# Kernel optimization log

Measured on AMD Instinct MI355X. Metric: run time of the kernel, lower is better.

## Reference

```python
import jax, jax.numpy as jnp
import numpy as np

# ---- dims / hyperparams (match init_kwargs) ----
D, B, S, NE, NC = 256, 4, 8192, 2048, 512
WIN, RK, TKE, TKC = 4, 4, 4, 4          # s window, route_topk, expanded_topk, compressed_topk
ALPHA, BS2B, BB2S = 1.0, 0.5, 0.5       # alpha_b, beta_s_to_b, beta_b_to_s
S_SC, B_SC, X_SC = 0.25, 0.2, 0.15      # s/b/cross delta scales
EPS = 1e-5
INV_SQRT_D = float(1.0 / np.sqrt(D))


def _ln(x, g, b):
    m = jnp.mean(x, -1, keepdims=True)
    v = jnp.mean(jnp.square(x - m), -1, keepdims=True)
    return (x - m) * jax.lax.rsqrt(v + EPS) * g + b


def _window_prop(state, val, w):
    # local window attention via diagonal-bilinear pairwise scores; never builds [S,S]
    n = state.shape[1]
    offs = jnp.arange(-WIN, WIN + 1)
    idx = jnp.arange(n)[:, None] + offs[None, :]            # [n, K]
    valid = (idx >= 0) & (idx < n)
    idxc = jnp.clip(idx, 0, n - 1)
    nb_s = state[:, idxc]                                    # [B, n, K, D]
    nb_v = val[:, idxc]
    sc = jnp.einsum('bnd,bnkd->bnk', state * w, nb_s) * INV_SQRT_D
    sc = jnp.where(valid, sc, -1e30)
    a = jax.nn.softmax(sc, axis=-1)
    return (jnp.einsum('bnk,bnkd->bnd', a, nb_s),
            jnp.einsum('bnk,bnkd->bnd', a, nb_v))


def _topk_prop(state, val, w, k):
    # global topk sparse attention over the (small) expanded/compressed node set
    sc = jnp.einsum('bnd,bmd->bnm', state * w, state) * INV_SQRT_D
    top, idx = jax.lax.top_k(sc, k)                          # [B, N, k]
    a = jax.nn.softmax(top, axis=-1)
    take = jax.vmap(lambda x, i: x[i])                       # gather rows per batch
    nb_s = take(state, idx)                                  # [B, N, k, D]
    nb_v = take(val, idx)
    return (jnp.einsum('bnk,bnkd->bnd', a, nb_s),
            jnp.einsum('bnk,bnkd->bnd', a, nb_v))


def _sparse_transition(src_s, src_v, W, bias, nd, k):
    # LinearRoute logits -> topk dst per src -> softmax weights -> scatter-add into dst
    logits = src_s @ W + bias                                # [B, Ns, Nd]
    top, idx = jax.lax.top_k(logits, k)
    wgt = jax.nn.softmax(top, axis=-1)                       # [B, Ns, k]

    def scat(i, ww, fs, fv):
        ii = i.reshape(-1)
        cs = (ww[..., None] * fs[:, None, :]).reshape(-1, fs.shape[-1])
        cv = (ww[..., None] * fv[:, None, :]).reshape(-1, fv.shape[-1])
        z = jnp.zeros((nd, fs.shape[-1]), fs.dtype)
        return z.at[ii].add(cs), z.at[ii].add(cv)

    return jax.vmap(scat)(idx, wgt, src_s, src_v)            # [B, Nd, D] x2


def _forward(s_state, s_val, w_pair_s, w_pair_e, w_pair_c,
             W_expand, b_expand, W_b2s, b_b2s, W_comp, b_comp, W_s2b, b_s2b,
             ln_g_s, ln_b_s, ln_g_e, ln_b_e, ln_g_c, ln_b_c):
    bsz = s_state.shape[0]
    # 1) sequence window propagation + stabilize
    ds, dv = _window_prop(s_state, s_val, w_pair_s)
    s_state = jnp.tanh(s_state + S_SC * ds)
    s_val = _ln(s_val + S_SC * dv, ln_g_s, ln_b_s)
    # 2) compressed layer bootstrapped from zeros (compressed_b=None) + stabilize
    c_state = jnp.zeros((bsz, NC, D), s_state.dtype)
    c_val = _ln(jnp.zeros((bsz, NC, D), s_state.dtype), ln_g_c, ln_b_c)
    # 3) expanded layer: expand transition then topk propagation + stabilize
    e_state = jnp.zeros((bsz, NE, D), s_state.dtype)
    e_val = jnp.zeros((bsz, NE, D), s_state.dtype)
    sc_b = ALPHA * B_SC
    ds, dv = _sparse_transition(c_state, c_val, W_expand, b_expand, NE, RK)
    e_state = e_state + sc_b * ds; e_val = e_val + sc_b * dv
    ds, dv = _topk_prop(e_state, e_val, w_pair_e, TKE)
    e_state = jnp.tanh(e_state + sc_b * ds)
    e_val = _ln(e_val + sc_b * dv, ln_g_e, ln_b_e)
    # 4) expanded -> sequence cross update + stabilize
    sc_x = ALPHA * BB2S * X_SC
    ds, dv = _sparse_transition(e_state, e_val, W_b2s, b_b2s, S, RK)
    s_state = jnp.tanh(s_state + sc_x * ds)
    s_val = _ln(s_val + sc_x * dv, ln_g_s, ln_b_s)
    # 5) next compressed: compress, s->b, compressed propagation + stabilize
    nc_state, nc_val = c_state, c_val
    ds, dv = _sparse_transition(e_state, e_val, W_comp, b_comp, NC, RK)
    nc_state = nc_state + sc_b * ds; nc_val = nc_val + sc_b * dv
    sc_sb = ALPHA * BS2B * X_SC
    ds, dv = _sparse_transition(s_state, s_val, W_s2b, b_s2b, NC, RK)
    nc_state = nc_state + sc_sb * ds; nc_val = nc_val + sc_sb * dv
    ds, dv = _topk_prop(nc_state, nc_val, w_pair_c, TKC)
    nc_state = jnp.tanh(nc_state + sc_b * ds)
    nc_val = _ln(nc_val + sc_b * dv, ln_g_c, ln_b_c)
    return (s_state, s_val, nc_state, nc_val)


def setup_inputs() -> dict:
    key = jax.random.key(0)
    ks = jax.random.split(key, 16)
    rs = float(1.0 / np.sqrt(D))
    return {
        's_state': jax.random.normal(ks[0], (B, S, D), jnp.float32),
        's_val': jax.random.normal(ks[1], (B, S, D), jnp.float32),
        'w_pair_s': jax.random.normal(ks[2], (D,), jnp.float32) * rs,
        'w_pair_e': jax.random.normal(ks[3], (D,), jnp.float32) * rs,
        'w_pair_c': jax.random.normal(ks[4], (D,), jnp.float32) * rs,
        'W_expand': jax.random.normal(ks[5], (D, NE), jnp.float32) * rs,
        'b_expand': jnp.zeros((NE,), jnp.float32),
        'W_b2s': jax.random.normal(ks[6], (D, S), jnp.float32) * rs,
        'b_b2s': jnp.zeros((S,), jnp.float32),
        'W_comp': jax.random.normal(ks[7], (D, NC), jnp.float32) * rs,
        'b_comp': jnp.zeros((NC,), jnp.float32),
        'W_s2b': jax.random.normal(ks[8], (D, NC), jnp.float32) * rs,
        'b_s2b': jnp.zeros((NC,), jnp.float32),
        'ln_g_s': jnp.ones((D,), jnp.float32), 'ln_b_s': jnp.zeros((D,), jnp.float32),
        'ln_g_e': jnp.ones((D,), jnp.float32), 'ln_b_e': jnp.zeros((D,), jnp.float32),
        'ln_g_c': jnp.ones((D,), jnp.float32), 'ln_b_c': jnp.zeros((D,), jnp.float32),
    }


def reference(s_state, s_val, w_pair_s, w_pair_e, w_pair_c,
              W_expand, b_expand, W_b2s, b_b2s, W_comp, b_comp, W_s2b, b_s2b,
              ln_g_s, ln_b_s, ln_g_e, ln_b_e, ln_g_c, ln_b_c):
    return _forward(s_state, s_val, w_pair_s, w_pair_e, w_pair_c,
                    W_expand, b_expand, W_b2s, b_b2s, W_comp, b_comp, W_s2b, b_s2b,
                    ln_g_s, ln_b_s, ln_g_e, ln_b_e, ln_g_c, ln_b_c)
```

## Files before the change

kernel.cpp:

```cpp
#include <hip/hip_runtime.h>
#include <math.h>

#define DD 256
#define BATCH 4
#define SEQ 8192
#define NEE 2048
#define NCC 512
#define EPSL 1e-5f
#define INV_SQRT_D 0.0625f

typedef __attribute__((ext_vector_type(8))) short short8;
typedef __attribute__((ext_vector_type(4))) float f32x4;

__device__ __forceinline__ float4 ld4(const float* p){ return *(const float4*)p; }
__device__ __forceinline__ void st4(float* p, const float4& v){ *(float4*)p = v; }
__device__ __forceinline__ void fma4(float4& a, float s, const float4& b){
  a.x = fmaf(s,b.x,a.x); a.y = fmaf(s,b.y,a.y); a.z = fmaf(s,b.z,a.z); a.w = fmaf(s,b.w,a.w);
}
__device__ __forceinline__ float4 tanh4(const float4& v){
  float4 r; r.x=tanhf(v.x); r.y=tanhf(v.y); r.z=tanhf(v.z); r.w=tanhf(v.w); return r;
}
__device__ __forceinline__ ushort f2bf(float x){
  unsigned u = __float_as_uint(x);
  unsigned r = u + 0x7fffu + ((u >> 16) & 1u);
  return (ushort)(r >> 16);
}
__device__ __forceinline__ float bf2f(ushort h){
  return __uint_as_float(((unsigned)h) << 16);
}

__device__ __forceinline__ bool t4_better(float v1, int i1, float v2, int i2){
  return (v1 > v2) || (v1 == v2 && i1 < i2);
}
__device__ __forceinline__ void t4_init(float* v, int* i){
#pragma unroll
  for (int k=0;k<4;k++){ v[k] = -INFINITY; i[k] = 0x7fffffff; }
}
__device__ __forceinline__ void t4_insert(float* v, int* i, float nv, int ni){
  if (t4_better(nv, ni, v[3], i[3])){
    v[3]=nv; i[3]=ni;
    if (t4_better(v[3],i[3],v[2],i[2])){ float tv=v[2]; v[2]=v[3]; v[3]=tv; int ti=i[2]; i[2]=i[3]; i[3]=ti;
      if (t4_better(v[2],i[2],v[1],i[1])){ tv=v[1]; v[1]=v[2]; v[2]=tv; ti=i[1]; i[1]=i[2]; i[2]=ti;
        if (t4_better(v[1],i[1],v[0],i[0])){ tv=v[0]; v[0]=v[1]; v[1]=tv; ti=i[0]; i[0]=i[1]; i[1]=ti; }
      }
    }
  }
}
__device__ __forceinline__ void t4_ce(float* v, int* i, int x, int y){
  if (t4_better(v[y],i[y],v[x],i[x])){ float tv=v[x]; v[x]=v[y]; v[y]=tv; int ti=i[x]; i[x]=i[y]; i[y]=ti; }
}
__device__ __forceinline__ void t4_merge(float* av, int* ai, const float* bv, const int* bi){
  float lv[4]; int li[4];
#pragma unroll
  for (int k=0;k<4;k++){
    if (t4_better(av[k],ai[k],bv[3-k],bi[3-k])){ lv[k]=av[k]; li[k]=ai[k]; }
    else { lv[k]=bv[3-k]; li[k]=bi[3-k]; }
  }
  t4_ce(lv,li,0,2); t4_ce(lv,li,1,3); t4_ce(lv,li,0,1); t4_ce(lv,li,2,3);
#pragma unroll
  for (int k=0;k<4;k++){ av[k]=lv[k]; ai[k]=li[k]; }
}
__device__ __forceinline__ void t4_wave_merge(float* v, int* i){
#pragma unroll
  for (int off=1; off<64; off<<=1){
    float bv[4]; int bi[4];
#pragma unroll
    for (int k=0;k<4;k++){ bv[k]=__shfl_xor(v[k],off); bi[k]=__shfl_xor(i[k],off); }
    t4_merge(v,i,bv,bi);
  }
}

__global__ __launch_bounds__(256) void k0_prep(
    const float* __restrict__ b_expand, const float* __restrict__ b_b2s, const float* __restrict__ b_comp,
    const float* __restrict__ ln_b_c, const float* __restrict__ ln_g_e, const float* __restrict__ ln_b_e,
    float* __restrict__ sumE, int* __restrict__ idxB2S, float* __restrict__ wgtB2S,
    int* __restrict__ idxComp, float* __restrict__ wgtComp)
{
  __shared__ int s_idx[3][4];
  __shared__ float s_wgt[3][4];
  __shared__ float red[16];
  int t = threadIdx.x, wv = t>>6, lane = t&63;
  if (wv < 3){
    const float* arr = (wv==0)? b_expand : (wv==1? b_b2s : b_comp);
    int n = (wv==0)? NEE : (wv==1? SEQ : NCC);
    float v[4]; int ix[4]; t4_init(v,ix);
    for (int m=lane; m<n; m+=64) t4_insert(v,ix, arr[m], m);
    t4_wave_merge(v,ix);
    if (lane==0){
      float e0=1.f, e1=expf(v[1]-v[0]), e2=expf(v[2]-v[0]), e3=expf(v[3]-v[0]);
      float inv = 1.f/(e0+e1+e2+e3);
      s_idx[wv][0]=ix[0]; s_idx[wv][1]=ix[1]; s_idx[wv][2]=ix[2]; s_idx[wv][3]=ix[3];
      s_wgt[wv][0]=e0*inv; s_wgt[wv][1]=e1*inv; s_wgt[wv][2]=e2*inv; s_wgt[wv][3]=e3*inv;
    }
  }
  __syncthreads();
  float c = ln_b_c[t];
  float cs = c, cq = c*c;
#pragma unroll
  for (int off=32; off; off>>=1){ cs += __shfl_xor(cs,off); cq += __shfl_xor(cq,off); }
  if (lane==0){ red[wv]=cs; red[8+wv]=cq; }
  __syncthreads();
  float mean_c = (red[0]+red[1]+red[2]+red[3]) * (1.f/256.f);
  float var_c  = (red[8]+red[9]+red[10]+red[11]) * (1.f/256.f) - mean_c*mean_c;
  float cm = c - mean_c;
  float g = ln_g_e[t], be = ln_b_e[t];
  float a[4]; float q = 0.f;
#pragma unroll
  for (int k=0;k<4;k++){
    a[k] = 0.2f * (float)NCC * s_wgt[0][k];
    if (s_idx[0][k] < 4) q += a[k];
  }
  q *= 0.25f;
  float se = 0.f;
#pragma unroll
  for (int k=0;k<4;k++){
    float tk = a[k] + 0.2f*q;
    se += tk*cm*rsqrtf(tk*tk*var_c + EPSL)*g + be;
  }
  float tz = 0.2f*q;
  se += (float)(NEE-4) * (tz*cm*rsqrtf(tz*tz*var_c + EPSL)*g + be);
  sumE[t] = se;
  if (t < 4){
    idxB2S[t] = s_idx[1][t]; wgtB2S[t] = s_wgt[1][t];
    idxComp[t] = s_idx[2][t]; wgtComp[t] = s_wgt[2][t];
  }
}

__global__ __launch_bounds__(256) void k1_window(
    const float* __restrict__ s_state, const float* __restrict__ s_val,
    const float* __restrict__ w_pair_s, const float* __restrict__ ln_g_s, const float* __restrict__ ln_b_s,
    const float* __restrict__ sumE, const int* __restrict__ idxB2S, const float* __restrict__ wgtB2S,
    float* __restrict__ out_state, float* __restrict__ out_val)
{
  int gw = (blockIdx.x << 2) + (threadIdx.x >> 6);
  int lane = threadIdx.x & 63;
  int b = gw >> 13, r = gw & (SEQ-1);
  size_t rowoff = ((size_t)gw) << 8;
  size_t bbase = ((size_t)b) << 21;
  int d0 = lane << 2;
  float4 x = ld4(s_state + rowoff + d0);
  float4 v = ld4(s_val + rowoff + d0);
  float4 wp = ld4(w_pair_s + d0);
  float qx=x.x*wp.x, qy=x.y*wp.y, qz=x.z*wp.z, qw=x.w*wp.w;
  float sc[9]; float4 ns[9];
#pragma unroll
  for (int k=0;k<9;k++){
    int rr = r + k - 4;
    int rc = rr < 0 ? 0 : (rr > SEQ-1 ? SEQ-1 : rr);
    ns[k] = ld4(s_state + bbase + (((size_t)rc)<<8) + d0);
    sc[k] = qx*ns[k].x + qy*ns[k].y + qz*ns[k].z + qw*ns[k].w;
  }
#pragma unroll
  for (int off=32; off; off>>=1){
#pragma unroll
    for (int k=0;k<9;k++) sc[k] += __shfl_xor(sc[k], off);
  }
  float mx = -INFINITY;
#pragma unroll
  for (int k=0;k<9;k++){
    int rr = r + k - 4;
    sc[k] = (rr>=0 && rr<SEQ) ? sc[k]*INV_SQRT_D : -1e30f;
    mx = fmaxf(mx, sc[k]);
  }
  float ssum = 0.f;
#pragma unroll
  for (int k=0;k<9;k++){ sc[k] = expf(sc[k]-mx); ssum += sc[k]; }
  float inv = 1.f/ssum;
  float4 ds = make_float4(0,0,0,0), dv = make_float4(0,0,0,0);
#pragma unroll
  for (int k=0;k<9;k++) fma4(ds, sc[k]*inv, ns[k]);
#pragma unroll
  for (int k=0;k<9;k++){
    int rr = r + k - 4;
    int rc = rr < 0 ? 0 : (rr > SEQ-1 ? SEQ-1 : rr);
    float4 nv = ld4(s_val + bbase + (((size_t)rc)<<8) + d0);
    fma4(dv, sc[k]*inv, nv);
  }
  float4 s1;
  s1.x = tanhf(x.x + 0.25f*ds.x); s1.y = tanhf(x.y + 0.25f*ds.y);
  s1.z = tanhf(x.z + 0.25f*ds.z); s1.w = tanhf(x.w + 0.25f*ds.w);
  st4(out_state + rowoff + d0, tanh4(s1));
  float4 y;
  y.x = v.x + 0.25f*dv.x; y.y = v.y + 0.25f*dv.y; y.z = v.z + 0.25f*dv.z; y.w = v.w + 0.25f*dv.w;
  float sm = y.x+y.y+y.z+y.w;
  float sq = y.x*y.x+y.y*y.y+y.z*y.z+y.w*y.w;
#pragma unroll
  for (int off=32; off; off>>=1){ sm += __shfl_xor(sm,off); sq += __shfl_xor(sq,off); }
  float mean = sm*(1.f/256.f);
  float rstd = rsqrtf(sq*(1.f/256.f) - mean*mean + EPSL);
  float4 g = ld4(ln_g_s + d0), be = ld4(ln_b_s + d0);
  float4 y1;
  y1.x = (y.x-mean)*rstd*g.x + be.x; y1.y = (y.y-mean)*rstd*g.y + be.y;
  y1.z = (y.z-mean)*rstd*g.z + be.z; y1.w = (y.w-mean)*rstd*g.w + be.w;
#pragma unroll
  for (int k=0;k<4;k++){
    if (r == idxB2S[k]){
      float cb = 0.075f * wgtB2S[k];
      float4 sE = ld4(sumE + d0);
      fma4(y1, cb, sE);
    }
  }
  sm = y1.x+y1.y+y1.z+y1.w;
  sq = y1.x*y1.x+y1.y*y1.y+y1.z*y1.z+y1.w*y1.w;
#pragma unroll
  for (int off=32; off; off>>=1){ sm += __shfl_xor(sm,off); sq += __shfl_xor(sq,off); }
  float mean2 = sm*(1.f/256.f);
  float rstd2 = rsqrtf(sq*(1.f/256.f) - mean2*mean2 + EPSL);
  float4 o;
  o.x = (y1.x-mean2)*rstd2*g.x + be.x; o.y = (y1.y-mean2)*rstd2*g.y + be.y;
  o.z = (y1.z-mean2)*rstd2*g.z + be.z; o.w = (y1.w-mean2)*rstd2*g.w + be.w;
  st4(out_val + rowoff + d0, o);
}

__global__ __launch_bounds__(256) void k2w_pack(const float* __restrict__ W,
    ushort* __restrict__ Whi, ushort* __restrict__ Wlo)
{
  int t = blockIdx.x*256 + threadIdx.x;
  int kb = t >> 11;
  int cf = (t >> 6) & 31;
  int l  = t & 63;
  int k0 = kb*32 + ((l>>4)<<3);
  int col = (cf<<4) + (l&15);
  size_t off = (size_t)t << 3;
#pragma unroll
  for (int j=0;j<8;j++){
    float x = W[(size_t)(k0+j)*NCC + col];
    ushort h = f2bf(x);
    Whi[off+j] = h;
    Wlo[off+j] = f2bf(x - bf2f(h));
  }
}

__global__ __launch_bounds__(256) void k2_mfma(
    const float* __restrict__ A, const ushort* __restrict__ Whi, const ushort* __restrict__ Wlo,
    const float* __restrict__ bias,
    int* __restrict__ topk_idx, float* __restrict__ topk_wgt, int* __restrict__ counts)
{
  __shared__ __align__(16) ushort Asp[2][32][264];
  __shared__ float mv[32][17];
  __shared__ int   mi[32][17];
  int tid = threadIdx.x;
  size_t row_base = (size_t)blockIdx.x * 32;
  {
    const float4* Ab = (const float4*)(A + row_base*DD);
#pragma unroll
    for (int i=0;i<8;i++){
      int q = i*256 + tid;
      int row = q >> 6, k4 = q & 63;
      float4 x = Ab[q];
      ushort4 h, lo;
      h.x = f2bf(x.x); h.y = f2bf(x.y); h.z = f2bf(x.z); h.w = f2bf(x.w);
      lo.x = f2bf(x.x - bf2f(h.x)); lo.y = f2bf(x.y - bf2f(h.y));
      lo.z = f2bf(x.z - bf2f(h.z)); lo.w = f2bf(x.w - bf2f(h.w));
      *(ushort4*)&Asp[0][row][k4*4] = h;
      *(ushort4*)&Asp[1][row][k4*4] = lo;
    }
  }
  __syncthreads();
  int w = tid >> 6, l = tid & 63;
  int lg = l >> 4, lr = l & 15;
  f32x4 acc[2][8];
#pragma unroll
  for (int rf=0; rf<2; rf++)
#pragma unroll
    for (int cf=0; cf<8; cf++) acc[rf][cf] = (f32x4){0.f,0.f,0.f,0.f};
  for (int kb=0; kb<8; kb++){
    short8 bh[8], bl[8];
#pragma unroll
    for (int cf=0; cf<8; cf++){
      int cfg = (w<<3) + cf;
      size_t off = (((size_t)(kb*32 + cfg) << 6) + l) << 3;
      bh[cf] = *(const short8*)(Whi + off);
      bl[cf] = *(const short8*)(Wlo + off);
    }
    short8 ah[2], al[2];
#pragma unroll
    for (int rf=0; rf<2; rf++){
      int row = (rf<<4) + lr;
      int k = kb*32 + (lg<<3);
      ah[rf] = *(const short8*)&Asp[0][row][k];
      al[rf] = *(const short8*)&Asp[1][row][k];
    }
#pragma unroll
    for (int cf=0; cf<8; cf++){
#pragma unroll
      for (int rf=0; rf<2; rf++){
        acc[rf][cf] = __builtin_amdgcn_mfma_f32_16x16x32_bf16(ah[rf], bh[cf], acc[rf][cf], 0, 0, 0);
        acc[rf][cf] = __builtin_amdgcn_mfma_f32_16x16x32_bf16(al[rf], bh[cf], acc[rf][cf], 0, 0, 0);
        acc[rf][cf] = __builtin_amdgcn_mfma_f32_16x16x32_bf16(ah[rf], bl[cf], acc[rf][cf], 0, 0, 0);
      }
    }
  }
  float bcol[8];
  int rel[8];
#pragma unroll
  for (int cf=0; cf<8; cf++){
    bcol[cf] = bias[(w<<7) + (cf<<4) + lr];
    rel[cf] = (cf<<4) + lr;
  }
#pragma unroll
  for (int rf=0; rf<2; rf++){
#pragma unroll
    for (int reg=0; reg<4; reg++){
      float av[8];
#pragma unroll
      for (int cf=0; cf<8; cf++) av[cf] = acc[rf][cf][reg] + bcol[cf];
      float tv4[4]; int tc4[4];
#pragma unroll
      for (int r=0; r<4; r++){
        float m = fmaxf(fmaxf(fmaxf(av[0],av[1]),fmaxf(av[2],av[3])),
                        fmaxf(fmaxf(av[4],av[5]),fmaxf(av[6],av[7])));
#pragma unroll
        for (int off=1; off<16; off<<=1) m = fmaxf(m, __shfl_xor(m, off));
        int cand = 0x7fffffff;
#pragma unroll
        for (int cf=7; cf>=0; cf--) cand = (av[cf]==m) ? rel[cf] : cand;
#pragma unroll
        for (int off=1; off<16; off<<=1) cand = min(cand, __shfl_xor(cand, off));
        tv4[r] = m; tc4[r] = cand;
        if (r < 3){
#pragma unroll
          for (int cf=0; cf<8; cf++) av[cf] = (rel[cf]==cand) ? -INFINITY : av[cf];
        }
      }
      if (lr == 0){
        int rowl = (rf<<4) + (lg<<2) + reg;
#pragma unroll
        for (int r=0; r<4; r++){ mv[rowl][(w<<2)+r] = tv4[r]; mi[rowl][(w<<2)+r] = (w<<7) + tc4[r]; }
      }
    }
  }
  __syncthreads();
  if (tid < 32){
    float v[4]; int ix[4]; t4_init(v, ix);
#pragma unroll
    for (int j=0; j<16; j++) t4_insert(v, ix, mv[tid][j], mi[tid][j]);
    float e0=1.f, e1=expf(v[1]-v[0]), e2=expf(v[2]-v[0]), e3=expf(v[3]-v[0]);
    float inv = 1.f/(e0+e1+e2+e3);
    size_t row = row_base + tid;
    int b = (int)(row >> 13);
    topk_idx[row*4+0]=ix[0]; topk_idx[row*4+1]=ix[1]; topk_idx[row*4+2]=ix[2]; topk_idx[row*4+3]=ix[3];
    topk_wgt[row*4+0]=e0*inv; topk_wgt[row*4+1]=e1*inv; topk_wgt[row*4+2]=e2*inv; topk_wgt[row*4+3]=e3*inv;
    atomicAdd(&counts[(b<<9)+ix[0]],1); atomicAdd(&counts[(b<<9)+ix[1]],1);
    atomicAdd(&counts[(b<<9)+ix[2]],1); atomicAdd(&counts[(b<<9)+ix[3]],1);
  }
}

__global__ void kz_zero(int* __restrict__ counts){
  int i = blockIdx.x*256 + threadIdx.x;
  if (i < BATCH*NCC) counts[i] = 0;
}

__global__ __launch_bounds__(256) void k3_scan(const int* __restrict__ counts,
    int* __restrict__ offsets, int* __restrict__ cursor)
{
  __shared__ int part[256];
  int t = threadIdx.x;
  int loc[8]; int s = 0;
#pragma unroll
  for (int i=0;i<8;i++){ loc[i] = counts[t*8+i]; s += loc[i]; }
  part[t] = s;
  __syncthreads();
  for (int off=1; off<256; off<<=1){
    int add = (t>=off)? part[t-off] : 0;
    __syncthreads();
    part[t] += add;
    __syncthreads();
  }
  int run = part[t] - s;
#pragma unroll
  for (int i=0;i<8;i++){ offsets[t*8+i] = run; cursor[t*8+i] = run; run += loc[i]; }
  if (t==255) offsets[BATCH*NCC] = run;
}

__global__ void k4_fill(const int* __restrict__ topk_idx, const float* __restrict__ topk_wgt,
    int* __restrict__ cursor, int* __restrict__ csr_src, float* __restrict__ csr_wgt)
{
  int row = blockIdx.x*256 + threadIdx.x;
  if (row >= BATCH*SEQ) return;
  int b = row >> 13, r = row & (SEQ-1);
#pragma unroll
  for (int k=0;k<4;k++){
    int dest = topk_idx[row*4+k];
    float wgt = topk_wgt[row*4+k];
    int pos = atomicAdd(&cursor[(b<<9)+dest], 1);
    csr_src[pos] = r;
    csr_wgt[pos] = 0.075f * wgt;
  }
}

__global__ __launch_bounds__(256) void k5_gather(
    const int* __restrict__ offsets, const int* __restrict__ csr_src, const float* __restrict__ csr_wgt,
    const float* __restrict__ st, const float* __restrict__ vl,
    const float* __restrict__ ln_b_c, const float* __restrict__ sumE,
    const int* __restrict__ idxComp, const float* __restrict__ wgtComp,
    float* __restrict__ ncs, float* __restrict__ ncv)
{
  int g = blockIdx.x;
  int b = g >> 9, dest = g & (NCC-1);
  int t = threadIdx.x;
  int i0 = offsets[g], i1 = offsets[g+1];
  const float* Sb = st + (((size_t)b)<<21);
  const float* Vb = vl + (((size_t)b)<<21);
  float accs = 0.f, accv = 0.f;
  for (int i=i0; i<i1; i++){
    int src = csr_src[i];
    float wg = csr_wgt[i];
    accs = fmaf(wg, Sb[((size_t)src<<8) + t], accs);
    accv = fmaf(wg, Vb[((size_t)src<<8) + t], accv);
  }
  float base = ln_b_c[t];
#pragma unroll
  for (int k=0;k<4;k++) if (dest == idxComp[k]) base = fmaf(0.2f*wgtComp[k], sumE[t], base);
  ncs[((size_t)g<<8) + t] = accs;
  ncv[((size_t)g<<8) + t] = base + accv;
}

__global__ __launch_bounds__(256) void k5t_transpose(const float* __restrict__ ncs, float* __restrict__ ncsT){
  __shared__ float tile[64][65];
  int b = blockIdx.z;
  int m0 = blockIdx.x*64, d0 = blockIdx.y*64;
  int tx = threadIdx.x & 63, ty = threadIdx.x >> 6;
  const float* src = ncs + (((size_t)b)<<17);
  for (int i=ty; i<64; i+=4) tile[i][tx] = src[(size_t)(m0+i)*DD + d0 + tx];
  __syncthreads();
  float* dst = ncsT + (((size_t)b)<<17);
  for (int i=ty; i<64; i+=4) dst[(size_t)(d0+i)*NCC + m0 + tx] = tile[tx][i];
}

__global__ __launch_bounds__(256) void k6_ncprop(
    const float* __restrict__ ncs, const float* __restrict__ ncv, const float* __restrict__ ncsT,
    const float* __restrict__ w_pair_c, const float* __restrict__ ln_g_c, const float* __restrict__ ln_b_c,
    float* __restrict__ o_ncs, float* __restrict__ o_ncv)
{
  __shared__ float Alds[256*13];
  int tid = threadIdx.x;
  int b = blockIdx.x >> 6;
  int n_base = (blockIdx.x & 63) << 3;
  const float* Sb = ncs + (((size_t)b)<<17);
  const float* Vb = ncv + (((size_t)b)<<17);
  const float* Tb = ncsT + (((size_t)b)<<17);
  float wc = w_pair_c[tid] * INV_SQRT_D;
#pragma unroll
  for (int i=0;i<8;i++) Alds[tid*13 + i] = Sb[(size_t)(n_base+i)*DD + tid] * wc;
  __syncthreads();
  int lane = tid & 63, rg = tid >> 6;
  int r0 = rg << 1, c0 = lane << 3;
  float acc[2][8];
#pragma unroll
  for (int j=0;j<2;j++)
#pragma unroll
    for (int c=0;c<8;c++) acc[j][c] = 0.f;
  for (int kk=0; kk<256; kk++){
    float4 w0 = ld4(Tb + (size_t)kk*NCC + c0);
    float4 w1 = ld4(Tb + (size_t)kk*NCC + c0 + 4);
    float a0 = Alds[kk*13 + r0];
    float a1 = Alds[kk*13 + r0 + 1];
    float wv_[8] = {w0.x,w0.y,w0.z,w0.w,w1.x,w1.y,w1.z,w1.w};
#pragma unroll
    for (int c=0;c<8;c++){
      acc[0][c] = fmaf(a0, wv_[c], acc[0][c]);
      acc[1][c] = fmaf(a1, wv_[c], acc[1][c]);
    }
  }
  int d0 = lane << 2;
  float4 g4 = ld4(ln_g_c + d0), be4 = ld4(ln_b_c + d0);
#pragma unroll
  for (int j=0;j<2;j++){
    float tv[4]; int ti[4]; t4_init(tv,ti);
#pragma unroll
    for (int c=0;c<8;c++) t4_insert(tv,ti, acc[j][c], c0+c);
    t4_wave_merge(tv,ti);
    float e0=1.f, e1=expf(tv[1]-tv[0]), e2=expf(tv[2]-tv[0]), e3=expf(tv[3]-tv[0]);
    float inv = 1.f/(e0+e1+e2+e3);
    float aw[4] = {e0*inv, e1*inv, e2*inv, e3*inv};
    int n = n_base + r0 + j;
    float4 stt = ld4(Sb + (size_t)n*DD + d0);
    float4 vv  = ld4(Vb + (size_t)n*DD + d0);
    float4 dsv = make_float4(0,0,0,0), dvv = make_float4(0,0,0,0);
#pragma unroll
    for (int k=0;k<4;k++){
      float4 ms = ld4(Sb + (size_t)ti[k]*DD + d0);
      float4 mv = ld4(Vb + (size_t)ti[k]*DD + d0);
      fma4(dsv, aw[k], ms); fma4(dvv, aw[k], mv);
    }
    float4 os;
    os.x = tanhf(stt.x + 0.2f*dsv.x); os.y = tanhf(stt.y + 0.2f*dsv.y);
    os.z = tanhf(stt.z + 0.2f*dsv.z); os.w = tanhf(stt.w + 0.2f*dsv.w);
    size_t orow = (((size_t)b)<<17) + ((size_t)n<<8);
    st4(o_ncs + orow + d0, os);
    float4 y;
    y.x = vv.x + 0.2f*dvv.x; y.y = vv.y + 0.2f*dvv.y;
    y.z = vv.z + 0.2f*dvv.z; y.w = vv.w + 0.2f*dvv.w;
    float sm = y.x+y.y+y.z+y.w;
    float sq = y.x*y.x+y.y*y.y+y.z*y.z+y.w*y.w;
#pragma unroll
    for (int off=32; off; off>>=1){ sm += __shfl_xor(sm,off); sq += __shfl_xor(sq,off); }
    float mean = sm*(1.f/256.f);
    float rstd = rsqrtf(sq*(1.f/256.f) - mean*mean + EPSL);
    float4 o;
    o.x = (y.x-mean)*rstd*g4.x + be4.x; o.y = (y.y-mean)*rstd*g4.y + be4.y;
    o.z = (y.z-mean)*rstd*g4.z + be4.z; o.w = (y.w-mean)*rstd*g4.w + be4.w;
    st4(o_ncv + orow + d0, o);
  }
}

extern "C" void kernel_launch(void* const* d_in, const int* in_sizes, int n_in,
                              void* d_out, int out_size, void* d_ws, size_t ws_size,
                              hipStream_t stream)
{
  const float* s_state = (const float*)d_in[0];
  const float* s_val   = (const float*)d_in[1];
  const float* w_pair_s= (const float*)d_in[2];
  const float* w_pair_c= (const float*)d_in[4];
  const float* b_expand= (const float*)d_in[6];
  const float* b_b2s   = (const float*)d_in[8];
  const float* b_comp  = (const float*)d_in[10];
  const float* W_s2b   = (const float*)d_in[11];
  const float* b_s2b   = (const float*)d_in[12];
  const float* ln_g_s  = (const float*)d_in[13];
  const float* ln_b_s  = (const float*)d_in[14];
  const float* ln_g_e  = (const float*)d_in[15];
  const float* ln_b_e  = (const float*)d_in[16];
  const float* ln_g_c  = (const float*)d_in[17];
  const float* ln_b_c  = (const float*)d_in[18];

  float* o_sstate = (float*)d_out;
  float* o_sval   = o_sstate + (size_t)BATCH*SEQ*DD;
  float* o_ncs    = o_sval + (size_t)BATCH*SEQ*DD;
  float* o_ncv    = o_ncs + (size_t)BATCH*NCC*DD;

  char* w = (char*)d_ws;
  float* sumE    = (float*)(w);
  int*   idxB2S  = (int*)(w + 1024);
  float* wgtB2S  = (float*)(w + 1040);
  int*   idxComp = (int*)(w + 1056);
  float* wgtComp = (float*)(w + 1072);
  int*   topk_idx= (int*)(w + 4096);
  float* topk_wgt= (float*)(w + 4096 + 524288);
  int*   counts  = (int*)(w + 1052672);
  int*   offsets = (int*)(w + 1069056);
  int*   cursor  = (int*)(w + 1085440);
  int*   csr_src = (int*)(w + 1101824);
  float* csr_wgt = (float*)(w + 1626112);
  float* ncs_ws  = (float*)(w + 2150400);
  float* ncv_ws  = ncs_ws + (size_t)BATCH*NCC*DD;
  float* ncsT_ws = ncv_ws + (size_t)BATCH*NCC*DD;
  ushort* wpk_hi = (ushort*)(w + 8441856);
  ushort* wpk_lo = (ushort*)(w + 8441856 + 262144);

  hipLaunchKernelGGL(k0_prep, dim3(1), dim3(256), 0, stream,
      b_expand, b_b2s, b_comp, ln_b_c, ln_g_e, ln_b_e, sumE, idxB2S, wgtB2S, idxComp, wgtComp);
  hipLaunchKernelGGL(k2w_pack, dim3(64), dim3(256), 0, stream, W_s2b, wpk_hi, wpk_lo);
  hipLaunchKernelGGL(k1_window, dim3(8192), dim3(256), 0, stream,
      s_state, s_val, w_pair_s, ln_g_s, ln_b_s, sumE, idxB2S, wgtB2S, o_sstate, o_sval);
  hipLaunchKernelGGL(kz_zero, dim3(8), dim3(256), 0, stream, counts);
  hipLaunchKernelGGL(k2_mfma, dim3(1024), dim3(256), 0, stream,
      o_sstate, wpk_hi, wpk_lo, b_s2b, topk_idx, topk_wgt, counts);
  hipLaunchKernelGGL(k3_scan, dim3(1), dim3(256), 0, stream, counts, offsets, cursor);
  hipLaunchKernelGGL(k4_fill, dim3(128), dim3(256), 0, stream,
      topk_idx, topk_wgt, cursor, csr_src, csr_wgt);
  hipLaunchKernelGGL(k5_gather, dim3(2048), dim3(256), 0, stream,
      offsets, csr_src, csr_wgt, o_sstate, o_sval, ln_b_c, sumE, idxComp, wgtComp, ncs_ws, ncv_ws);
  hipLaunchKernelGGL(k5t_transpose, dim3(8,4,BATCH), dim3(256), 0, stream, ncs_ws, ncsT_ws);
  hipLaunchKernelGGL(k6_ncprop, dim3(256), dim3(256), 0, stream,
      ncs_ws, ncv_ws, ncsT_ws, w_pair_c, ln_g_c, ln_b_c, o_ncs, o_ncv);
}
```

Measured before the change: 417.3 us.

## Software-pipeline W fragment loads in k2_mfma with register double buffering

Restructures the k2_mfma inner loop so the packed hi/lo weight fragments are fetched in groups of two column tiles into alternating register buffers. The next group's global loads are issued before the current group's MFMAs, with sched_barrier fencing the order. The first group is prefetched before the A-tile conversion, and the lo weights are addressed by a fixed offset from the hi pointer instead of a separate argument. A launch_bounds occupancy hint of 4 is added to cap register use, which risks spilling or scheduling constraints in exchange for hiding global load latency behind matrix ops.

```diff
diff --git a/kernel.cpp b/kernel.cpp
--- a/kernel.cpp
+++ b/kernel.cpp
@@ -231,8 +231,8 @@
   }
 }
 
-__global__ __launch_bounds__(256) void k2_mfma(
-    const float* __restrict__ A, const ushort* __restrict__ Whi, const ushort* __restrict__ Wlo,
+__global__ __launch_bounds__(256, 4) void k2_mfma(
+    const float* __restrict__ A, const ushort* __restrict__ Whi,
     const float* __restrict__ bias,
     int* __restrict__ topk_idx, float* __restrict__ topk_wgt, int* __restrict__ counts)
 {
@@ -241,6 +241,34 @@
   __shared__ int   mi[32][17];
   int tid = threadIdx.x;
   size_t row_base = (size_t)blockIdx.x * 32;
+  int w = tid >> 6, l = tid & 63;
+  int lg = l >> 4, lr = l & 15;
+  const ushort* pw = Whi + ((w<<12) + (l<<3));
+
+#define LOADG(KB, G, DST) { \
+    const ushort* _p = pw + (KB)*16384 + (G)*1024; \
+    DST[0] = *(const short8*)_p; \
+    DST[2] = *(const short8*)(_p + 512); \
+    DST[1] = *(const short8*)(_p + 131072); \
+    DST[3] = *(const short8*)(_p + 131072 + 512); }
+
+#define COMPG(G, B) { \
+    int _c0 = (G)<<1, _c1 = _c0+1; \
+    acc[0][_c0] = __builtin_amdgcn_mfma_f32_16x16x32_bf16(ah0, B[0], acc[0][_c0], 0,0,0); \
+    acc[1][_c0] = __builtin_amdgcn_mfma_f32_16x16x32_bf16(ah1, B[0], acc[1][_c0], 0,0,0); \
+    acc[0][_c1] = __builtin_amdgcn_mfma_f32_16x16x32_bf16(ah0, B[2], acc[0][_c1], 0,0,0); \
+    acc[1][_c1] = __builtin_amdgcn_mfma_f32_16x16x32_bf16(ah1, B[2], acc[1][_c1], 0,0,0); \
+    acc[0][_c0] = __builtin_amdgcn_mfma_f32_16x16x32_bf16(al0, B[0], acc[0][_c0], 0,0,0); \
+    acc[1][_c0] = __builtin_amdgcn_mfma_f32_16x16x32_bf16(al1, B[0], acc[1][_c0], 0,0,0); \
+    acc[0][_c0] = __builtin_amdgcn_mfma_f32_16x16x32_bf16(ah0, B[1], acc[0][_c0], 0,0,0); \
+    acc[1][_c0] = __builtin_amdgcn_mfma_f32_16x16x32_bf16(ah1, B[1], acc[1][_c0], 0,0,0); \
+    acc[0][_c1] = __builtin_amdgcn_mfma_f32_16x16x32_bf16(al0, B[2], acc[0][_c1], 0,0,0); \
+    acc[1][_c1] = __builtin_amdgcn_mfma_f32_16x16x32_bf16(al1, B[2], acc[1][_c1], 0,0,0); \
+    acc[0][_c1] = __builtin_amdgcn_mfma_f32_16x16x32_bf16(ah0, B[3], acc[0][_c1], 0,0,0); \
+    acc[1][_c1] = __builtin_amdgcn_mfma_f32_16x16x32_bf16(ah1, B[3], acc[1][_c1], 0,0,0); }
+
+  short8 bA[4], bB[4];
+  LOADG(0, 0, bA);
   {
     const float4* Ab = (const float4*)(A + row_base*DD);
 #pragma unroll
@@ -257,40 +285,33 @@
     }
   }
   __syncthreads();
-  int w = tid >> 6, l = tid & 63;
-  int lg = l >> 4, lr = l & 15;
   f32x4 acc[2][8];
 #pragma unroll
   for (int rf=0; rf<2; rf++)
 #pragma unroll
     for (int cf=0; cf<8; cf++) acc[rf][cf] = (f32x4){0.f,0.f,0.f,0.f};
+#pragma unroll 1
   for (int kb=0; kb<8; kb++){
-    short8 bh[8], bl[8];
-#pragma unroll
-    for (int cf=0; cf<8; cf++){
-      int cfg = (w<<3) + cf;
-      size_t off = (((size_t)(kb*32 + cfg) << 6) + l) << 3;
-      bh[cf] = *(const short8*)(Whi + off);
-      bl[cf] = *(const short8*)(Wlo + off);
-    }
-    short8 ah[2], al[2];
-#pragma unroll
-    for (int rf=0; rf<2; rf++){
-      int row = (rf<<4) + lr;
-      int k = kb*32 + (lg<<3);
-      ah[rf] = *(const short8*)&Asp[0][row][k];
-      al[rf] = *(const short8*)&Asp[1][row][k];
-    }
-#pragma unroll
-    for (int cf=0; cf<8; cf++){
-#pragma unroll
-      for (int rf=0; rf<2; rf++){
-        acc[rf][cf] = __builtin_amdgcn_mfma_f32_16x16x32_bf16(ah[rf], bh[cf], acc[rf][cf], 0, 0, 0);
-        acc[rf][cf] = __builtin_amdgcn_mfma_f32_16x16x32_bf16(al[rf], bh[cf], acc[rf][cf], 0, 0, 0);
-        acc[rf][cf] = __builtin_amdgcn_mfma_f32_16x16x32_bf16(ah[rf], bl[cf], acc[rf][cf], 0, 0, 0);
-      }
-    }
-  }
+    int ka = kb*32 + (lg<<3);
+    short8 ah0 = *(const short8*)&Asp[0][lr][ka];
+    short8 ah1 = *(const short8*)&Asp[0][16+lr][ka];
+    short8 al0 = *(const short8*)&Asp[1][lr][ka];
+    short8 al1 = *(const short8*)&Asp[1][16+lr][ka];
+    LOADG(kb, 1, bB);
+    __builtin_amdgcn_sched_barrier(0);
+    COMPG(0, bA);
+    LOADG(kb, 2, bA);
+    __builtin_amdgcn_sched_barrier(0);
+    COMPG(1, bB);
+    LOADG(kb, 3, bB);
+    __builtin_amdgcn_sched_barrier(0);
+    COMPG(2, bA);
+    if (kb < 7) LOADG(kb+1, 0, bA);
+    __builtin_amdgcn_sched_barrier(0);
+    COMPG(3, bB);
+  }
+#undef LOADG
+#undef COMPG
   float bcol[8];
   int rel[8];
 #pragma unroll
@@ -556,7 +577,7 @@
       s_state, s_val, w_pair_s, ln_g_s, ln_b_s, sumE, idxB2S, wgtB2S, o_sstate, o_sval);
   hipLaunchKernelGGL(kz_zero, dim3(8), dim3(256), 0, stream, counts);
   hipLaunchKernelGGL(k2_mfma, dim3(1024), dim3(256), 0, stream,
-      o_sstate, wpk_hi, wpk_lo, b_s2b, topk_idx, topk_wgt, counts);
+      o_sstate, wpk_hi, b_s2b, topk_idx, topk_wgt, counts);
   hipLaunchKernelGGL(k3_scan, dim3(1), dim3(256), 0, stream, counts, offsets, cursor);
   hipLaunchKernelGGL(k4_fill, dim3(128), dim3(256), 0, stream,
       topk_idx, topk_wgt, cursor, csr_src, csr_wgt);
```

Result: no change. 420.0 us (+0.6%).
